# Optimization experiments

Hardware: AMD Instinct MI355X
Metric: run time of the kernel (lower is better)

The kernel has to match this reference:

```python
import jax, jax.numpy as jnp
import numpy as np

N = 10000      # nodes
E = 80000      # edges
D = 128        # d_model
H = 8          # num_heads
DH = 128       # d_head
DFF = 512      # d_ff
CLAMP = 5.0
EPS = 1e-5


def setup_inputs() -> dict:
    key = jax.random.key(0)
    ks = jax.random.split(key, 10)
    s = 0.05
    return {
        "feat": jax.random.normal(ks[0], (N, D), jnp.float32),
        "src": jax.random.randint(ks[1], (E,), 0, N),
        "dst": jax.random.randint(ks[2], (E,), 0, N),
        # projections stored as (in, out); x @ W == torch Linear(bias=False)
        "Wq": jax.random.normal(ks[3], (D, H * DH), jnp.float32) * s,
        "Wk": jax.random.normal(ks[4], (D, H * DH), jnp.float32) * s,
        "Wv": jax.random.normal(ks[5], (D, H * DH), jnp.float32) * s,
        "Wo": jax.random.normal(ks[6], (H * DH, D), jnp.float32) * s,
        "g1": jnp.ones((D,), jnp.float32),
        "b1": jnp.zeros((D,), jnp.float32),
        "W1": jax.random.normal(ks[7], (D, DFF), jnp.float32) * s,
        "bf1": jnp.zeros((DFF,), jnp.float32),
        "W2": jax.random.normal(ks[8], (DFF, D), jnp.float32) * s,
        "bf2": jnp.zeros((D,), jnp.float32),
        "g2": jnp.ones((D,), jnp.float32),
        "b2": jnp.zeros((D,), jnp.float32),
    }


def _layer_norm(x, g, b):
    mu = x.mean(-1, keepdims=True)
    xc = x - mu
    var = (xc * xc).mean(-1, keepdims=True)
    return xc * jax.lax.rsqrt(var + EPS) * g + b


def reference(feat, src, dst, Wq, Wk, Wv, Wo, g1, b1, W1, bf1, W2, bf2, g2, b2):
    h_src = feat[src]                              # (E, D) gather
    h_dst = feat[dst]                              # (E, D)
    q = (h_dst @ Wq).reshape(E, H, DH)             # query from destination node
    k = (h_src @ Wk).reshape(E, H, DH)
    v = (h_src @ Wv).reshape(E, H, DH)
    # per-edge logits: QK dot per head, scale, clamp
    u = jnp.clip((q * k).sum(-1) / np.sqrt(DH), -CLAMP, CLAMP)  # (E, H)
    # edge_softmax over incoming edges of each destination node
    m = jax.ops.segment_max(u, dst, num_segments=N)             # (N, H)
    ex = jnp.exp(u - m[dst])
    den = jax.ops.segment_sum(ex, dst, num_segments=N)          # (N, H)
    a = ex / den[dst]                                           # (E, H)
    # weighted V, segment-sum to destination nodes
    agg = jax.ops.segment_sum(a[..., None] * v, dst, num_segments=N)  # (N, H, DH)
    uh = _layer_norm(feat + agg.reshape(N, H * DH) @ Wo, g1, b1)
    ffn = jax.nn.relu(uh @ W1 + bf1) @ W2 + bf2
    return _layer_norm(uh + ffn, g2, b2)
```

## Files before the change

### kernel.cpp

```cpp
#include <hip/hip_runtime.h>

typedef unsigned int uint;
typedef unsigned short ushort;
typedef __attribute__((ext_vector_type(8))) short short8;
typedef __attribute__((ext_vector_type(4))) float f32x4;

#define DEV static __device__ __forceinline__

DEV float bf_lo(uint v) { return __uint_as_float(v << 16); }
DEV float bf_hi(uint v) { return __uint_as_float(v & 0xffff0000u); }
DEV ushort f2bf(float f) {
    uint u = __float_as_uint(f);
    u += 0x7fffu + ((u >> 16) & 1u);
    return (ushort)(u >> 16);
}
DEV void stC(float* p, float v) { *p = v; }
DEV void stC(ushort* p, float v) { *p = f2bf(v); }

template <typename OT>
DEV void transp_body(float (*tile)[65], const float* __restrict__ in,
                     OT* __restrict__ out, int R, int C, int bid, int t)
{
    const int nbx = C >> 6;
    const int bx = bid % nbx, by = bid / nbx;
#pragma unroll
    for (int it = 0; it < 4; ++it) {
        int idx = it * 256 + t;
        int rr = idx >> 4, cc4 = (idx & 15) * 4;
        float4 v = *reinterpret_cast<const float4*>(in + (size_t)(by * 64 + rr) * C + bx * 64 + cc4);
        tile[cc4][rr] = v.x; tile[cc4 + 1][rr] = v.y;
        tile[cc4 + 2][rr] = v.z; tile[cc4 + 3][rr] = v.w;
    }
    __syncthreads();
#pragma unroll
    for (int it = 0; it < 4; ++it) {
        int idx = it * 256 + t;
        int cc = idx >> 4, rr4 = (idx & 15) * 4;
        OT* po = out + (size_t)(bx * 64 + cc) * R + by * 64 + rr4;
        if constexpr (__is_same(OT, float)) {
            float4 o = { tile[cc][rr4], tile[cc][rr4 + 1], tile[cc][rr4 + 2], tile[cc][rr4 + 3] };
            *reinterpret_cast<float4*>(po) = o;
        } else {
            ushort4 o = { f2bf(tile[cc][rr4]), f2bf(tile[cc][rr4 + 1]),
                          f2bf(tile[cc][rr4 + 2]), f2bf(tile[cc][rr4 + 3]) };
            *reinterpret_cast<ushort4*>(po) = o;
        }
    }
}

__global__ __launch_bounds__(256) void prep1_kernel(
    int4* __restrict__ cntd4, int nz,
    const float* __restrict__ feat, ushort* __restrict__ featbf,
    const float* __restrict__ Wo, float* __restrict__ WoT,
    const float* __restrict__ W1, ushort* __restrict__ W1T,
    const float* __restrict__ W2, ushort* __restrict__ W2T, int N)
{
    __shared__ float tile[64][65];
    const int zb = (nz + 255) / 256;
    const int nf = (N * 32 + 255) / 256;
    const int b = blockIdx.x, t = threadIdx.x;
    if (b < zb) {
        int i = b * 256 + t;
        if (i < nz) cntd4[i] = int4{0, 0, 0, 0};
    } else if (b < zb + nf) {
        int i = (b - zb) * 256 + t;
        if (i >= N * 32) return;
        float4 v = reinterpret_cast<const float4*>(feat)[i];
        ushort4 o;
        o.x = f2bf(v.x); o.y = f2bf(v.y); o.z = f2bf(v.z); o.w = f2bf(v.w);
        reinterpret_cast<ushort4*>(featbf)[i] = o;
    } else if (b < zb + nf + 32) {
        transp_body<float>(tile, Wo, WoT, 1024, 128, b - zb - nf, t);
    } else if (b < zb + nf + 48) {
        transp_body<ushort>(tile, W1, W1T, 128, 512, b - zb - nf - 32, t);
    } else {
        transp_body<ushort>(tile, W2, W2T, 512, 128, b - zb - nf - 48, t);
    }
}

__global__ __launch_bounds__(256) void hist_mpt_kernel(
    const int* __restrict__ dst, int* __restrict__ cntd, int E, int eb,
    const float* __restrict__ Wq, const float* __restrict__ Wk,
    const float* __restrict__ Wv, const float* __restrict__ WoT,
    ushort* __restrict__ MPT)
{
    __shared__ char lds[65536];
    const int b = blockIdx.x, t = threadIdx.x;
    if (b < eb) {
        int e = b * 256 + t;
        if (e < E) atomicAdd(&cntd[dst[e]], 1);
        return;
    }
    char* As = lds;
    char* Bs = lds + 32768;

    const int mb = b - eb;
    const int part = mb >> 3, h = mb & 7;
    const int lane = t & 63, w = t >> 6;
    const int frow = lane & 15, kgrp = lane >> 4;

    const float* Asrc = part ? WoT : Wk;
    const float* Bsrc = part ? Wv : Wq;
    const float ascale = part ? 1.f : 0.08838834764831845f;

#pragma unroll
    for (int it = 0; it < 16; ++it) {
        int idx = it * 256 + t;
        int r = idx >> 5, c4 = (idx & 31) * 4;
        size_t goff = (size_t)r * 1024 + h * 128 + c4;
        float4 va = *reinterpret_cast<const float4*>(Asrc + goff);
        ushort4 ua = { f2bf(va.x * ascale), f2bf(va.y * ascale),
                       f2bf(va.z * ascale), f2bf(va.w * ascale) };
        *reinterpret_cast<ushort4*>(&As[r * 256 + ((c4 * 2) ^ ((r & 7) << 4))]) = ua;
        float4 vb = *reinterpret_cast<const float4*>(Bsrc + goff);
        ushort4 ub = { f2bf(vb.x), f2bf(vb.y), f2bf(vb.z), f2bf(vb.w) };
        *reinterpret_cast<ushort4*>(&Bs[r * 256 + ((c4 * 2) ^ ((r & 7) << 4))]) = ub;
    }
    __syncthreads();

    f32x4 acc[2][8] = {};
#pragma unroll
    for (int ks = 0; ks < 4; ++ks) {
        int koff = ks * 64 + kgrp * 16;
        short8 bfr[8];
#pragma unroll
        for (int fn = 0; fn < 8; ++fn) {
            int col = fn * 16 + frow;
            bfr[fn] = *reinterpret_cast<const short8*>(&Bs[col * 256 + (koff ^ ((col & 7) << 4))]);
        }
#pragma unroll
        for (int fm = 0; fm < 2; ++fm) {
            int row = w * 32 + fm * 16 + frow;
            short8 a = *reinterpret_cast<const short8*>(&As[row * 256 + (koff ^ ((row & 7) << 4))]);
#pragma unroll
            for (int fn = 0; fn < 8; ++fn)
                acc[fm][fn] = __builtin_amdgcn_mfma_f32_16x16x32_bf16(a, bfr[fn], acc[fm][fn], 0, 0, 0);
        }
    }

    const size_t base = ((size_t)part * 1024 + h * 128) * 128;
#pragma unroll
    for (int fm = 0; fm < 2; ++fm)
#pragma unroll
        for (int fn = 0; fn < 8; ++fn)
#pragma unroll
            for (int r = 0; r < 4; ++r) {
                int j = w * 32 + fm * 16 + kgrp * 4 + r;
                int i = fn * 16 + frow;
                MPT[base + (size_t)j * 128 + i] = f2bf(acc[fm][fn][r]);
            }
}

__global__ __launch_bounds__(1024) void scan1_kernel(
    const int* __restrict__ cntd, int* __restrict__ offd, int* __restrict__ curd, int N)
{
    __shared__ int ls[1024];
    const int t = threadIdx.x;
    const int chunk = (N + 1023) >> 10;
    int base = t * chunk;
    int s = 0;
    for (int i = 0; i < chunk; ++i) {
        int idx = base + i;
        if (idx < N) s += cntd[idx];
    }
    ls[t] = s;
    __syncthreads();
    for (int d = 1; d < 1024; d <<= 1) {
        int v = (t >= d) ? ls[t - d] : 0;
        __syncthreads();
        ls[t] += v;
        __syncthreads();
    }
    int run = t ? ls[t - 1] : 0;
    for (int i = 0; i < chunk; ++i) {
        int idx = base + i;
        if (idx < N) {
            offd[idx] = run;
            curd[idx] = run;
            run += cntd[idx];
        }
    }
    if (t == 1023) offd[N] = run;
}

__global__ __launch_bounds__(256) void gvo_scat_kernel(
    const ushort* __restrict__ A, const ushort* __restrict__ BT,
    ushort* __restrict__ C, int M, int nbg,
    const int* __restrict__ src, const int* __restrict__ dst,
    int* __restrict__ curd, int* __restrict__ src_d, int E)
{
    __shared__ char lds[32768];
    const int b = blockIdx.x, t = threadIdx.x;

    if (b >= nbg) {
        int e = (b - nbg) * 256 + t;
        if (e >= E) return;
        int s = src[e], d = dst[e];
        int pd = atomicAdd(&curd[d], 1);
        src_d[pd] = s;
        return;
    }

    char* AsB = lds;
    char* BsB = lds + 16384;
    const int m0 = (b >> 4) * 128;
    const int n0 = (b & 15) * 128;
    const int lane = t & 63, wid = t >> 6;
    const int wm = wid >> 1, wn = wid & 1;
    const int frow = lane & 15, kgrp = lane >> 4;

    f32x4 acc[4][4] = {};

    for (int kk = 0; kk < 128; kk += 64) {
#pragma unroll
        for (int it = 0; it < 4; ++it) {
            int q = it * 256 + t;
            int r = q >> 3, c8 = (q & 7) * 8;
            int gm = m0 + r;
            short8 v = {};
            if (gm < M) v = *reinterpret_cast<const short8*>(&A[(size_t)gm * 128 + kk + c8]);
            *reinterpret_cast<short8*>(&AsB[r * 128 + ((c8 * 2) ^ ((r & 7) << 4))]) = v;
        }
#pragma unroll
        for (int it = 0; it < 4; ++it) {
            int q = it * 256 + t;
            int r = q >> 3, c8 = (q & 7) * 8;
            short8 v = *reinterpret_cast<const short8*>(&BT[(size_t)(n0 + r) * 128 + kk + c8]);
            *reinterpret_cast<short8*>(&BsB[r * 128 + ((c8 * 2) ^ ((r & 7) << 4))]) = v;
        }
        __syncthreads();
#pragma unroll
        for (int kp = 0; kp < 2; ++kp) {
            const int koffb = kp * 64 + kgrp * 16;
            short8 bb[4];
#pragma unroll
            for (int fn = 0; fn < 4; ++fn) {
                int col = wn * 64 + fn * 16 + frow;
                bb[fn] = *reinterpret_cast<const short8*>(&BsB[col * 128 + (koffb ^ ((col & 7) << 4))]);
            }
#pragma unroll
            for (int fm = 0; fm < 4; ++fm) {
                int row = wm * 64 + fm * 16 + frow;
                short8 a = *reinterpret_cast<const short8*>(&AsB[row * 128 + (koffb ^ ((row & 7) << 4))]);
#pragma unroll
                for (int fn = 0; fn < 4; ++fn)
                    acc[fm][fn] = __builtin_amdgcn_mfma_f32_16x16x32_bf16(a, bb[fn], acc[fm][fn], 0, 0, 0);
            }
        }
        __syncthreads();
    }

#pragma unroll
    for (int fm = 0; fm < 4; ++fm)
#pragma unroll
        for (int fn = 0; fn < 4; ++fn)
#pragma unroll
            for (int r = 0; r < 4; ++r) {
                int gm = m0 + wm * 64 + fm * 16 + kgrp * 4 + r;
                int gn = n0 + wn * 64 + fn * 16 + frow;
                if (gm >= M) continue;
                stC(&C[(size_t)gm * 2048 + gn], acc[fm][fn][r]);
            }
}

__global__ __launch_bounds__(256) void edge_fused_kernel(
    const ushort* __restrict__ featbf, const ushort* __restrict__ GVO,
    const int* __restrict__ src_d, const int* __restrict__ offd,
    const float* __restrict__ feat, const float* __restrict__ g1,
    const float* __restrict__ b1, float* __restrict__ uh,
    ushort* __restrict__ uhbf, int N)
{
    __shared__ float exl[4][16][8];
    __shared__ int   srcl[4][16];

    const int t = threadIdx.x;
    const int lane = t & 63, wid = t >> 6;
    const int frow = lane & 15, kgrp = lane >> 4;
    const int d = blockIdx.x * 4 + wid;
    if (d >= N) return;
    const int lo = offd[d], hi = offd[d + 1];
    const int deg = hi - lo;

    short8 afr[4];
#pragma unroll
    for (int ks = 0; ks < 4; ++ks)
        afr[ks] = *reinterpret_cast<const short8*>(
            &GVO[(size_t)d * 2048 + frow * 128 + ks * 32 + kgrp * 8]);

    float acch0[8] = {}, acch1[8] = {};
    float den_acc[4] = {};

    for (int tb = 0; tb < deg; tb += 16) {
        int ei = tb + frow;
        int sv = (ei < deg) ? src_d[lo + ei] : 0;

        f32x4 c = {};
#pragma unroll
        for (int ks = 0; ks < 4; ++ks) {
            short8 bfr = *reinterpret_cast<const short8*>(
                &featbf[(size_t)sv * 128 + ks * 32 + kgrp * 8]);
            c = __builtin_amdgcn_mfma_f32_16x16x32_bf16(afr[ks], bfr, c, 0, 0, 0);
        }

        float exr[4];
#pragma unroll
        for (int r = 0; r < 4; ++r) {
            float u = fminf(fmaxf(c[r], -5.f), 5.f);
            exr[r] = __expf(u);
        }
        if (kgrp < 2)
            *reinterpret_cast<float4*>(&exl[wid][frow][kgrp * 4]) =
                float4{exr[0], exr[1], exr[2], exr[3]};
        if (kgrp == 0) srcl[wid][frow] = sv;
#pragma unroll
        for (int r = 0; r < 4; ++r) {
            float v = (ei < deg) ? exr[r] : 0.f;
            v += __shfl_xor(v, 1); v += __shfl_xor(v, 2);
            v += __shfl_xor(v, 4); v += __shfl_xor(v, 8);
            den_acc[r] += v;
        }

        int vc = min(16, deg - tb);
        for (int i = 0; i < vc; ++i) {
            int s = srcl[wid][i];
            float4 e0 = *reinterpret_cast<const float4*>(&exl[wid][i][0]);
            float4 e1 = *reinterpret_cast<const float4*>(&exl[wid][i][4]);
            const uint* vrow = reinterpret_cast<const uint*>(GVO + (size_t)s * 2048 + 1024);
            uint gv0 = vrow[lane],       gv1 = vrow[64 + lane];
            uint gv2 = vrow[128 + lane], gv3 = vrow[192 + lane];
            uint gv4 = vrow[256 + lane], gv5 = vrow[320 + lane];
            uint gv6 = vrow[384 + lane], gv7 = vrow[448 + lane];
            acch0[0] += e0.x * bf_lo(gv0); acch1[0] += e0.x * bf_hi(gv0);
            acch0[1] += e0.y * bf_lo(gv1); acch1[1] += e0.y * bf_hi(gv1);
            acch0[2] += e0.z * bf_lo(gv2); acch1[2] += e0.z * bf_hi(gv2);
            acch0[3] += e0.w * bf_lo(gv3); acch1[3] += e0.w * bf_hi(gv3);
            acch0[4] += e1.x * bf_lo(gv4); acch1[4] += e1.x * bf_hi(gv4);
            acch0[5] += e1.y * bf_lo(gv5); acch1[5] += e1.y * bf_hi(gv5);
            acch0[6] += e1.z * bf_lo(gv6); acch1[6] += e1.z * bf_hi(gv6);
            acch0[7] += e1.w * bf_lo(gv7); acch1[7] += e1.w * bf_hi(gv7);
        }
    }

    float acc0 = 0.f, acc1 = 0.f;
#pragma unroll
    for (int h = 0; h < 8; ++h) {
        float dh = __shfl(den_acc[h & 3], (h & 4) << 2);
        float rd = (dh > 0.f) ? 1.f / dh : 0.f;
        acc0 += acch0[h] * rd;
        acc1 += acch1[h] * rd;
    }

    float2 v = reinterpret_cast<const float2*>(feat)[(size_t)d * 64 + lane];
    v.x += acc0;
    v.y += acc1;
    float sum = v.x + v.y;
#pragma unroll
    for (int off = 32; off; off >>= 1) sum += __shfl_xor(sum, off);
    float mean = sum * (1.f / 128.f);
    float cx = v.x - mean, cy = v.y - mean;
    float vs = cx * cx + cy * cy;
#pragma unroll
    for (int off = 32; off; off >>= 1) vs += __shfl_xor(vs, off);
    float r = rsqrtf(vs * (1.f / 128.f) + 1e-5f);
    float2 gg = reinterpret_cast<const float2*>(g1)[lane];
    float2 bb = reinterpret_cast<const float2*>(b1)[lane];
    float2 o;
    o.x = cx * r * gg.x + bb.x;
    o.y = cy * r * gg.y + bb.y;
    reinterpret_cast<float2*>(uh)[(size_t)d * 64 + lane] = o;
    ushort2 ob; ob.x = f2bf(o.x); ob.y = f2bf(o.y);
    reinterpret_cast<ushort2*>(uhbf)[(size_t)d * 64 + lane] = ob;
}

template <int NTILE, typename OT, bool BIAS, bool RELU, bool RES>
__global__ __launch_bounds__(256) void gemm_mfma(
    const ushort* __restrict__ A, const ushort* __restrict__ BT,
    const float* __restrict__ bias, const float* __restrict__ res,
    OT* __restrict__ C, int M, int K, int NC)
{
    constexpr int FN = NTILE * 2;
    constexpr int WN = NTILE * 32;
    __shared__ char lds[16384 + NTILE * 8192];
    char* AsB = lds;
    char* BsB = lds + 16384;

    const int m0 = blockIdx.y * 128;
    const int n0 = blockIdx.x * (NTILE * 64);
    const int t = threadIdx.x;
    const int lane = t & 63, wid = t >> 6;
    const int wm = wid >> 1, wn = wid & 1;
    const int frow = lane & 15, kgrp = lane >> 4;

    f32x4 acc[4][FN] = {};

    for (int kk = 0; kk < K; kk += 64) {
#pragma unroll
        for (int it = 0; it < 4; ++it) {
            int q = it * 256 + t;
            int r = q >> 3, c8 = (q & 7) * 8;
            int gm = m0 + r;
            short8 v = {};
            if (gm < M) v = *reinterpret_cast<const short8*>(&A[(size_t)gm * K + kk + c8]);
            *reinterpret_cast<short8*>(&AsB[r * 128 + ((c8 * 2) ^ ((r & 7) << 4))]) = v;
        }
#pragma unroll
        for (int it = 0; it < 2 * NTILE; ++it) {
            int q = it * 256 + t;
            int r = q >> 3, c8 = (q & 7) * 8;
            short8 v = *reinterpret_cast<const short8*>(&BT[(size_t)(n0 + r) * K + kk + c8]);
            *reinterpret_cast<short8*>(&BsB[r * 128 + ((c8 * 2) ^ ((r & 7) << 4))]) = v;
        }
        __syncthreads();
#pragma unroll
        for (int kp = 0; kp < 2; ++kp) {
            const int koffb = kp * 64 + kgrp * 16;
            short8 b[FN];
#pragma unroll
            for (int fn = 0; fn < FN; ++fn) {
                int col = wn * WN + fn * 16 + frow;
                b[fn] = *reinterpret_cast<const short8*>(&BsB[col * 128 + (koffb ^ ((col & 7) << 4))]);
            }
#pragma unroll
            for (int fm = 0; fm < 4; ++fm) {
                int row = wm * 64 + fm * 16 + frow;
                short8 a = *reinterpret_cast<const short8*>(&AsB[row * 128 + (koffb ^ ((row & 7) << 4))]);
#pragma unroll
                for (int fn = 0; fn < FN; ++fn)
                    acc[fm][fn] = __builtin_amdgcn_mfma_f32_16x16x32_bf16(a, b[fn], acc[fm][fn], 0, 0, 0);
            }
        }
        __syncthreads();
    }

#pragma unroll
    for (int fm = 0; fm < 4; ++fm)
#pragma unroll
        for (int fn = 0; fn < FN; ++fn)
#pragma unroll
            for (int r = 0; r < 4; ++r) {
                int gm = m0 + wm * 64 + fm * 16 + kgrp * 4 + r;
                int gn = n0 + wn * WN + fn * 16 + frow;
                if (gm >= M) continue;
                float v = acc[fm][fn][r];
                if (BIAS) v += bias[gn];
                if (RELU) v = fmaxf(v, 0.f);
                if (RES) v += res[(size_t)gm * NC + gn];
                stC(&C[(size_t)gm * NC + gn], v);
            }
}

__global__ __launch_bounds__(256) void gemm_mfma64(
    const ushort* __restrict__ A, const ushort* __restrict__ BT,
    const float* __restrict__ bias, const float* __restrict__ res,
    float* __restrict__ C, int M, int K, int NC)
{
    __shared__ char lds[16384];
    char* AsB = lds;
    char* BsB = lds + 8192;

    const int m0 = blockIdx.y * 64;
    const int n0 = blockIdx.x * 64;
    const int t = threadIdx.x;
    const int lane = t & 63, wid = t >> 6;
    const int wm = wid >> 1, wn = wid & 1;
    const int frow = lane & 15, kgrp = lane >> 4;

    f32x4 acc[2][2] = {};

    for (int kk = 0; kk < K; kk += 64) {
#pragma unroll
        for (int it = 0; it < 2; ++it) {
            int q = it * 256 + t;
            int r = q >> 3, c8 = (q & 7) * 8;
            int gm = m0 + r;
            short8 v = {};
            if (gm < M) v = *reinterpret_cast<const short8*>(&A[(size_t)gm * K + kk + c8]);
            *reinterpret_cast<short8*>(&AsB[r * 128 + ((c8 * 2) ^ ((r & 7) << 4))]) = v;
        }
#pragma unroll
        for (int it = 0; it < 2; ++it) {
            int q = it * 256 + t;
            int r = q >> 3, c8 = (q & 7) * 8;
            short8 v = *reinterpret_cast<const short8*>(&BT[(size_t)(n0 + r) * K + kk + c8]);
            *reinterpret_cast<short8*>(&BsB[r * 128 + ((c8 * 2) ^ ((r & 7) << 4))]) = v;
        }
        __syncthreads();
#pragma unroll
        for (int kp = 0; kp < 2; ++kp) {
            const int koffb = kp * 64 + kgrp * 16;
            short8 b[2];
#pragma unroll
            for (int fn = 0; fn < 2; ++fn) {
                int col = wn * 32 + fn * 16 + frow;
                b[fn] = *reinterpret_cast<const short8*>(&BsB[col * 128 + (koffb ^ ((col & 7) << 4))]);
            }
#pragma unroll
            for (int fm = 0; fm < 2; ++fm) {
                int row = wm * 32 + fm * 16 + frow;
                short8 a = *reinterpret_cast<const short8*>(&AsB[row * 128 + (koffb ^ ((row & 7) << 4))]);
#pragma unroll
                for (int fn = 0; fn < 2; ++fn)
                    acc[fm][fn] = __builtin_amdgcn_mfma_f32_16x16x32_bf16(a, b[fn], acc[fm][fn], 0, 0, 0);
            }
        }
        __syncthreads();
    }

#pragma unroll
    for (int fm = 0; fm < 2; ++fm)
#pragma unroll
        for (int fn = 0; fn < 2; ++fn)
#pragma unroll
            for (int r = 0; r < 4; ++r) {
                int gm = m0 + wm * 32 + fm * 16 + kgrp * 4 + r;
                int gn = n0 + wn * 32 + fn * 16 + frow;
                if (gm >= M) continue;
                float v = acc[fm][fn][r] + bias[gn] + res[(size_t)gm * NC + gn];
                C[(size_t)gm * NC + gn] = v;
            }
}

__global__ __launch_bounds__(256) void ln_kernel(
    const float* __restrict__ x, const float* __restrict__ g,
    const float* __restrict__ b, float* __restrict__ out, int M)
{
    int row = (int)((blockIdx.x * 256 + threadIdx.x) >> 6);
    int lane = threadIdx.x & 63;
    if (row >= M) return;
    float2 v = reinterpret_cast<const float2*>(x)[(size_t)row * 64 + lane];
    float sum = v.x + v.y;
#pragma unroll
    for (int off = 32; off; off >>= 1) sum += __shfl_xor(sum, off);
    float mean = sum * (1.f / 128.f);
    float cx = v.x - mean, cy = v.y - mean;
    float vs = cx * cx + cy * cy;
#pragma unroll
    for (int off = 32; off; off >>= 1) vs += __shfl_xor(vs, off);
    float r = rsqrtf(vs * (1.f / 128.f) + 1e-5f);
    float2 gg = reinterpret_cast<const float2*>(g)[lane];
    float2 bb = reinterpret_cast<const float2*>(b)[lane];
    float2 o;
    o.x = cx * r * gg.x + bb.x;
    o.y = cy * r * gg.y + bb.y;
    reinterpret_cast<float2*>(out)[(size_t)row * 64 + lane] = o;
}

extern "C" void kernel_launch(void* const* d_in, const int* in_sizes, int n_in,
                              void* d_out, int out_size, void* d_ws, size_t ws_size,
                              hipStream_t stream)
{
    const float* feat = (const float*)d_in[0];
    const int*   src  = (const int*)d_in[1];
    const int*   dst  = (const int*)d_in[2];
    const float* Wq   = (const float*)d_in[3];
    const float* Wk   = (const float*)d_in[4];
    const float* Wv   = (const float*)d_in[5];
    const float* Wo   = (const float*)d_in[6];
    const float* g1   = (const float*)d_in[7];
    const float* b1   = (const float*)d_in[8];
    const float* W1   = (const float*)d_in[9];
    const float* bf1  = (const float*)d_in[10];
    const float* W2   = (const float*)d_in[11];
    const float* bf2  = (const float*)d_in[12];
    const float* g2   = (const float*)d_in[13];
    const float* b2   = (const float*)d_in[14];
    const int N = in_sizes[0] / 128;
    const int E = in_sizes[1];
    float* out = (float*)d_out;

    char* w = (char*)d_ws;
    auto alloc = [&](size_t bytes) {
        char* p = w;
        w += (bytes + 255) & ~(size_t)255;
        return p;
    };
    ushort* MPT    = (ushort*)alloc((size_t)2048 * 128 * 2);
    float*  WoT    = (float*)alloc((size_t)128 * 1024 * 4);
    ushort* W1T    = (ushort*)alloc((size_t)512 * 128 * 2);
    ushort* W2T    = (ushort*)alloc((size_t)128 * 512 * 2);
    ushort* featbf = (ushort*)alloc((size_t)N * 128 * 2);
    ushort* GVO    = (ushort*)alloc((size_t)N * 2048 * 2);
    int*    cntd   = (int*)alloc((size_t)((N + 3) & ~3) * 4);
    int*    offd   = (int*)alloc((size_t)(N + 1) * 4);
    int*    curd   = (int*)alloc((size_t)N * 4);
    int*    src_d  = (int*)alloc((size_t)E * 4);
    float*  uh     = (float*)alloc((size_t)N * 128 * 4);
    ushort* uhbf   = (ushort*)alloc((size_t)N * 128 * 2);
    ushort* f1     = (ushort*)alloc((size_t)N * 512 * 2);
    float*  pre2   = (float*)alloc((size_t)N * 128 * 4);

    int nz = (N + 3) / 4;
    int zb = (nz + 255) / 256;
    int nf = (N * 32 + 255) / 256;
    prep1_kernel<<<zb + nf + 64, 256, 0, stream>>>(
        (int4*)cntd, nz, feat, featbf, Wo, WoT, W1, W1T, W2, W2T, N);

    int eb = (E + 255) / 256;
    hist_mpt_kernel<<<eb + 16, 256, 0, stream>>>(
        dst, cntd, E, eb, Wq, Wk, Wv, WoT, MPT);

    scan1_kernel<<<1, 1024, 0, stream>>>(cntd, offd, curd, N);

    int nbg = 16 * ((N + 127) / 128);
    gvo_scat_kernel<<<nbg + eb, 256, 0, stream>>>(
        featbf, MPT, GVO, N, nbg, src, dst, curd, src_d, E);

    edge_fused_kernel<<<(N + 3) / 4, 256, 0, stream>>>(
        featbf, GVO, src_d, offd, feat, g1, b1, uh, uhbf, N);

    dim3 f1_grid(512 / 128, (N + 127) / 128);
    gemm_mfma<2, ushort, true, true, false><<<f1_grid, 256, 0, stream>>>(
        uhbf, W1T, bf1, nullptr, f1, N, 128, 512);
    dim3 f2_grid(128 / 64, (N + 63) / 64);
    gemm_mfma64<<<f2_grid, 256, 0, stream>>>(
        f1, W2T, bf2, uh, pre2, N, 512, 128);
    int nwaves_n = (N * 64 + 255) / 256;
    ln_kernel<<<nwaves_n, 256, 0, stream>>>(pre2, g2, b2, out, N);
}
```

Before: 123.7 us.

## Aggregate raw source features per head and apply Wv·Wo projection after aggregation

Previously a per-node precomputed GVO table held both Q·K-fused rows and per-head V·Wo projected rows (2048 bf16 per node), and the edge kernel gathered 1024 projected values per edge. The new version keeps only the query-side G (1024 per node), gathers the 128-wide source feature row per edge, accumulates per-head weighted feature sums Y (N x 1024), then applies the fused Wv·Wo matrix with a separate GEMM and layer-norm kernel. This cuts the per-node GEMM output and per-edge gather traffic by moving projection after aggregation, at the cost of an extra N x 1024 x 128 GEMM, an intermediate Y buffer and two more kernel launches.

After: 127.5 us. 3.1% more time.

```diff
diff --git a/kernel.cpp b/kernel.cpp
--- a/kernel.cpp
+++ b/kernel.cpp
@@ -82,7 +82,7 @@
     const int* __restrict__ dst, int* __restrict__ cntd, int E, int eb,
     const float* __restrict__ Wq, const float* __restrict__ Wk,
     const float* __restrict__ Wv, const float* __restrict__ WoT,
-    ushort* __restrict__ MPT)
+    ushort* __restrict__ MG, ushort* __restrict__ PT)
 {
     __shared__ char lds[65536];
     const int b = blockIdx.x, t = threadIdx.x;
@@ -138,7 +138,6 @@
         }
     }
 
-    const size_t base = ((size_t)part * 1024 + h * 128) * 128;
 #pragma unroll
     for (int fm = 0; fm < 2; ++fm)
 #pragma unroll
@@ -147,7 +146,10 @@
             for (int r = 0; r < 4; ++r) {
                 int j = w * 32 + fm * 16 + kgrp * 4 + r;
                 int i = fn * 16 + frow;
-                MPT[base + (size_t)j * 128 + i] = f2bf(acc[fm][fn][r]);
+                if (part == 0)
+                    MG[((size_t)h * 128 + j) * 128 + i] = f2bf(acc[fm][fn][r]);
+                else
+                    PT[(size_t)j * 1024 + h * 128 + i] = f2bf(acc[fm][fn][r]);
             }
 }
 
@@ -203,8 +205,8 @@
 
     char* AsB = lds;
     char* BsB = lds + 16384;
-    const int m0 = (b >> 4) * 128;
-    const int n0 = (b & 15) * 128;
+    const int m0 = (b >> 3) * 128;
+    const int n0 = (b & 7) * 128;
     const int lane = t & 63, wid = t >> 6;
     const int wm = wid >> 1, wn = wid & 1;
     const int frow = lane & 15, kgrp = lane >> 4;
@@ -259,16 +261,14 @@
                 int gm = m0 + wm * 64 + fm * 16 + kgrp * 4 + r;
                 int gn = n0 + wn * 64 + fn * 16 + frow;
                 if (gm >= M) continue;
-                stC(&C[(size_t)gm * 2048 + gn], acc[fm][fn][r]);
+                stC(&C[(size_t)gm * 1024 + gn], acc[fm][fn][r]);
             }
 }
 
 __global__ __launch_bounds__(256) void edge_fused_kernel(
-    const ushort* __restrict__ featbf, const ushort* __restrict__ GVO,
+    const ushort* __restrict__ featbf, const ushort* __restrict__ G,
     const int* __restrict__ src_d, const int* __restrict__ offd,
-    const float* __restrict__ feat, const float* __restrict__ g1,
-    const float* __restrict__ b1, float* __restrict__ uh,
-    ushort* __restrict__ uhbf, int N)
+    ushort* __restrict__ Y, int N)
 {
     __shared__ float exl[4][16][8];
     __shared__ int   srcl[4][16];
@@ -285,9 +285,9 @@
 #pragma unroll
     for (int ks = 0; ks < 4; ++ks)
         afr[ks] = *reinterpret_cast<const short8*>(
-            &GVO[(size_t)d * 2048 + frow * 128 + ks * 32 + kgrp * 8]);
-
-    float acch0[8] = {}, acch1[8] = {};
+            &G[(size_t)d * 1024 + frow * 128 + ks * 32 + kgrp * 8]);
+
+    float y[16] = {};
     float den_acc[4] = {};
 
     for (int tb = 0; tb < deg; tb += 16) {
@@ -325,51 +325,28 @@
             int s = srcl[wid][i];
             float4 e0 = *reinterpret_cast<const float4*>(&exl[wid][i][0]);
             float4 e1 = *reinterpret_cast<const float4*>(&exl[wid][i][4]);
-            const uint* vrow = reinterpret_cast<const uint*>(GVO + (size_t)s * 2048 + 1024);
-            uint gv0 = vrow[lane],       gv1 = vrow[64 + lane];
-            uint gv2 = vrow[128 + lane], gv3 = vrow[192 + lane];
-            uint gv4 = vrow[256 + lane], gv5 = vrow[320 + lane];
-            uint gv6 = vrow[384 + lane], gv7 = vrow[448 + lane];
-            acch0[0] += e0.x * bf_lo(gv0); acch1[0] += e0.x * bf_hi(gv0);
-            acch0[1] += e0.y * bf_lo(gv1); acch1[1] += e0.y * bf_hi(gv1);
-            acch0[2] += e0.z * bf_lo(gv2); acch1[2] += e0.z * bf_hi(gv2);
-            acch0[3] += e0.w * bf_lo(gv3); acch1[3] += e0.w * bf_hi(gv3);
-            acch0[4] += e1.x * bf_lo(gv4); acch1[4] += e1.x * bf_hi(gv4);
-            acch0[5] += e1.y * bf_lo(gv5); acch1[5] += e1.y * bf_hi(gv5);
-            acch0[6] += e1.z * bf_lo(gv6); acch1[6] += e1.z * bf_hi(gv6);
-            acch0[7] += e1.w * bf_lo(gv7); acch1[7] += e1.w * bf_hi(gv7);
-        }
-    }
-
-    float acc0 = 0.f, acc1 = 0.f;
+            uint fv = reinterpret_cast<const uint*>(featbf)[(size_t)s * 64 + lane];
+            float fx = bf_lo(fv), fy = bf_hi(fv);
+            y[0]  += e0.x * fx; y[1]  += e0.x * fy;
+            y[2]  += e0.y * fx; y[3]  += e0.y * fy;
+            y[4]  += e0.z * fx; y[5]  += e0.z * fy;
+            y[6]  += e0.w * fx; y[7]  += e0.w * fy;
+            y[8]  += e1.x * fx; y[9]  += e1.x * fy;
+            y[10] += e1.y * fx; y[11] += e1.y * fy;
+            y[12] += e1.z * fx; y[13] += e1.z * fy;
+            y[14] += e1.w * fx; y[15] += e1.w * fy;
+        }
+    }
+
 #pragma unroll
     for (int h = 0; h < 8; ++h) {
         float dh = __shfl(den_acc[h & 3], (h & 4) << 2);
         float rd = (dh > 0.f) ? 1.f / dh : 0.f;
-        acc0 += acch0[h] * rd;
-        acc1 += acch1[h] * rd;
-    }
-
-    float2 v = reinterpret_cast<const float2*>(feat)[(size_t)d * 64 + lane];
-    v.x += acc0;
-    v.y += acc1;
-    float sum = v.x + v.y;
-#pragma unroll
-    for (int off = 32; off; off >>= 1) sum += __shfl_xor(sum, off);
-    float mean = sum * (1.f / 128.f);
-    float cx = v.x - mean, cy = v.y - mean;
-    float vs = cx * cx + cy * cy;
-#pragma unroll
-    for (int off = 32; off; off >>= 1) vs += __shfl_xor(vs, off);
-    float r = rsqrtf(vs * (1.f / 128.f) + 1e-5f);
-    float2 gg = reinterpret_cast<const float2*>(g1)[lane];
-    float2 bb = reinterpret_cast<const float2*>(b1)[lane];
-    float2 o;
-    o.x = cx * r * gg.x + bb.x;
-    o.y = cy * r * gg.y + bb.y;
-    reinterpret_cast<float2*>(uh)[(size_t)d * 64 + lane] = o;
-    ushort2 ob; ob.x = f2bf(o.x); ob.y = f2bf(o.y);
-    reinterpret_cast<ushort2*>(uhbf)[(size_t)d * 64 + lane] = ob;
+        ushort2 o;
+        o.x = f2bf(y[2 * h] * rd);
+        o.y = f2bf(y[2 * h + 1] * rd);
+        reinterpret_cast<ushort2*>(Y)[(size_t)d * 512 + h * 64 + lane] = o;
+    }
 }
 
 template <int NTILE, typename OT, bool BIAS, bool RELU, bool RES>
@@ -449,6 +426,7 @@
             }
 }
 
+template <bool BIAS>
 __global__ __launch_bounds__(256) void gemm_mfma64(
     const ushort* __restrict__ A, const ushort* __restrict__ BT,
     const float* __restrict__ bias, const float* __restrict__ res,
@@ -515,14 +493,17 @@
                 int gm = m0 + wm * 32 + fm * 16 + kgrp * 4 + r;
                 int gn = n0 + wn * 32 + fn * 16 + frow;
                 if (gm >= M) continue;
-                float v = acc[fm][fn][r] + bias[gn] + res[(size_t)gm * NC + gn];
+                float v = acc[fm][fn][r] + res[(size_t)gm * NC + gn];
+                if (BIAS) v += bias[gn];
                 C[(size_t)gm * NC + gn] = v;
             }
 }
 
+template <bool BFOUT>
 __global__ __launch_bounds__(256) void ln_kernel(
     const float* __restrict__ x, const float* __restrict__ g,
-    const float* __restrict__ b, float* __restrict__ out, int M)
+    const float* __restrict__ b, float* __restrict__ out,
+    ushort* __restrict__ outbf, int M)
 {
     int row = (int)((blockIdx.x * 256 + threadIdx.x) >> 6);
     int lane = threadIdx.x & 63;
@@ -543,6 +524,10 @@
     o.x = cx * r * gg.x + bb.x;
     o.y = cy * r * gg.y + bb.y;
     reinterpret_cast<float2*>(out)[(size_t)row * 64 + lane] = o;
+    if (BFOUT) {
+        ushort2 ob; ob.x = f2bf(o.x); ob.y = f2bf(o.y);
+        reinterpret_cast<ushort2*>(outbf)[(size_t)row * 64 + lane] = ob;
+    }
 }
 
 extern "C" void kernel_launch(void* const* d_in, const int* in_sizes, int n_in,
@@ -574,16 +559,19 @@
         w += (bytes + 255) & ~(size_t)255;
         return p;
     };
-    ushort* MPT    = (ushort*)alloc((size_t)2048 * 128 * 2);
+    ushort* MG     = (ushort*)alloc((size_t)1024 * 128 * 2);
+    ushort* PT     = (ushort*)alloc((size_t)128 * 1024 * 2);
     float*  WoT    = (float*)alloc((size_t)128 * 1024 * 4);
     ushort* W1T    = (ushort*)alloc((size_t)512 * 128 * 2);
     ushort* W2T    = (ushort*)alloc((size_t)128 * 512 * 2);
     ushort* featbf = (ushort*)alloc((size_t)N * 128 * 2);
-    ushort* GVO    = (ushort*)alloc((size_t)N * 2048 * 2);
+    ushort* G      = (ushort*)alloc(((size_t)N * 1024 + 2048) * 2);
+    ushort* Y      = (ushort*)alloc((size_t)N * 1024 * 2);
     int*    cntd   = (int*)alloc((size_t)((N + 3) & ~3) * 4);
     int*    offd   = (int*)alloc((size_t)(N + 1) * 4);
     int*    curd   = (int*)alloc((size_t)N * 4);
     int*    src_d  = (int*)alloc((size_t)E * 4);
+    float*  pre1   = (float*)alloc((size_t)N * 128 * 4);
     float*  uh     = (float*)alloc((size_t)N * 128 * 4);
     ushort* uhbf   = (ushort*)alloc((size_t)N * 128 * 2);
     ushort* f1     = (ushort*)alloc((size_t)N * 512 * 2);
@@ -597,23 +585,29 @@
 
     int eb = (E + 255) / 256;
     hist_mpt_kernel<<<eb + 16, 256, 0, stream>>>(
-        dst, cntd, E, eb, Wq, Wk, Wv, WoT, MPT);
+        dst, cntd, E, eb, Wq, Wk, Wv, WoT, MG, PT);
 
     scan1_kernel<<<1, 1024, 0, stream>>>(cntd, offd, curd, N);
 
-    int nbg = 16 * ((N + 127) / 128);
+    int nbg = 8 * ((N + 127) / 128);
     gvo_scat_kernel<<<nbg + eb, 256, 0, stream>>>(
-        featbf, MPT, GVO, N, nbg, src, dst, curd, src_d, E);
+        featbf, MG, G, N, nbg, src, dst, curd, src_d, E);
 
     edge_fused_kernel<<<(N + 3) / 4, 256, 0, stream>>>(
-        featbf, GVO, src_d, offd, feat, g1, b1, uh, uhbf, N);
+        featbf, G, src_d, offd, Y, N);
+
+    dim3 yg_grid(128 / 64, (N + 63) / 64);
+    gemm_mfma64<false><<<yg_grid, 256, 0, stream>>>(
+        Y, PT, nullptr, feat, pre1, N, 1024, 128);
+
+    int nwaves_n = (N * 64 + 255) / 256;
+    ln_kernel<true><<<nwaves_n, 256, 0, stream>>>(pre1, g1, b1, uh, uhbf, N);
 
     dim3 f1_grid(512 / 128, (N + 127) / 128);
     gemm_mfma<2, ushort, true, true, false><<<f1_grid, 256, 0, stream>>>(
         uhbf, W1T, bf1, nullptr, f1, N, 128, 512);
     dim3 f2_grid(128 / 64, (N + 63) / 64);
-    gemm_mfma64<<<f2_grid, 256, 0, stream>>>(
+    gemm_mfma64<true><<<f2_grid, 256, 0, stream>>>(
         f1, W2T, bf2, uh, pre2, N, 512, 128);
-    int nwaves_n = (N * 64 + 255) / 256;
-    ln_kernel<<<nwaves_n, 256, 0, stream>>>(pre2, g2, b2, out, N);
-}
+    ln_kernel<false><<<nwaves_n, 256, 0, stream>>>(pre2, g2, b2, out, nullptr, N);
+}
```
